# Kernel tuning notes

Hardware: AMD Instinct MI355X
Metric: run time of the kernel (lower is better)

Reference implementation:

```python
import jax, jax.numpy as jnp
import numpy as np

EMBED_DIM = 128
WINDOW_SIZE = 128
B, S, D = 2, 2048, EMBED_DIM
NEG_INF = -1e9


def setup_inputs() -> dict:
    key = jax.random.key(0)
    kq, kk, kv = jax.random.split(key, 3)
    q = jax.random.normal(kq, (B, S, D), dtype=jnp.float32)
    k = jax.random.normal(kk, (B, S, D), dtype=jnp.float32)
    v = jax.random.normal(kv, (B, S, D), dtype=jnp.float32)
    return {"q": q, "k": k, "v": v}


def reference(q, k, v):
    # Sliding-window causal attention: token i attends to [i-W, i] inclusive.
    Bq, Sq, Dq = q.shape
    W = WINDOW_SIZE
    scale = Dq ** -0.5
    offsets = jnp.arange(-W, 1)                      # [W+1]
    idx = jnp.arange(Sq)[:, None] + offsets[None, :]  # [S, W+1]
    valid = idx >= 0                                  # mask out-of-range (pre-sequence) keys
    idx_c = jnp.clip(idx, 0, Sq - 1)
    k_win = k[:, idx_c]                               # [B, S, W+1, D]
    v_win = v[:, idx_c]                               # [B, S, W+1, D]
    scores = jnp.einsum('bsd,bswd->bsw', q, k_win) * scale
    scores = jnp.where(valid[None, :, :], scores, NEG_INF)
    attn = jax.nn.softmax(scores, axis=-1)            # [B, S, W+1]
    out = jnp.einsum('bsw,bswd->bsd', attn, v_win)    # [B, S, D]
    return out
```

## Files before the change

### kernel.cpp

```cpp
#include <hip/hip_runtime.h>
#include <hip/hip_bf16.h>
#include <math.h>

#define SEQ 2048
#define DIME 128
#define BQ 16
#define NEG_INF -1.0e9f

typedef __attribute__((ext_vector_type(8))) short bf16x8;
typedef __attribute__((ext_vector_type(4))) float f32x4;

static __device__ __forceinline__ short cvt(float x) {
  __hip_bfloat16 h(x);
  return __builtin_bit_cast(short, h);
}

static __device__ __forceinline__ bf16x8 pack8(const float4 lo, const float4 hi) {
  bf16x8 f;
  f[0] = cvt(lo.x); f[1] = cvt(lo.y); f[2] = cvt(lo.z); f[3] = cvt(lo.w);
  f[4] = cvt(hi.x); f[5] = cvt(hi.y); f[6] = cvt(hi.z); f[7] = cvt(hi.w);
  return f;
}

__global__ __launch_bounds__(256) void swa_kernel(
    const float* __restrict__ q, const float* __restrict__ k,
    const float* __restrict__ v, float* __restrict__ out) {
  __shared__ float P[16][180];
  __shared__ float mW[9][16];
  __shared__ float sW[9][16];

  const int tid = threadIdx.x;
  const int lane = tid & 63;
  const int w = tid >> 6;
  const int col = lane & 15;
  const int g = lane >> 4;

  const int blk = blockIdx.x;
  const int b = blk >> 7;
  const int qs = (blk & 127) * BQ;
  const int kbase = qs - 128;

  const float* __restrict__ qb = q + (size_t)b * SEQ * DIME;
  const float* __restrict__ kb = k + (size_t)b * SEQ * DIME;
  const float* __restrict__ vb = v + (size_t)b * SEQ * DIME;

  float4 qlo[4], qhi[4];
  {
    const float* qrow = qb + (size_t)(qs + col) * DIME + 8 * g;
#pragma unroll
    for (int kc = 0; kc < 4; ++kc) {
      qlo[kc] = *(const float4*)(qrow + 32 * kc);
      qhi[kc] = *(const float4*)(qrow + 32 * kc + 4);
    }
  }

  float4 kraw[3][8];
#pragma unroll
  for (int ti = 0; ti < 2; ++ti) {
    const int t = 2 * w + ti;
    int krow = kbase + 16 * t + col;
    krow = krow < 0 ? 0 : krow;
    const float* krp = kb + (size_t)krow * DIME + 8 * g;
#pragma unroll
    for (int kc = 0; kc < 4; ++kc) {
      kraw[ti][2 * kc]     = *(const float4*)(krp + 32 * kc);
      kraw[ti][2 * kc + 1] = *(const float4*)(krp + 32 * kc + 4);
    }
  }
  if (w == 0) {
    const int krow = kbase + 16 * 8 + col;
    const float* krp = kb + (size_t)krow * DIME + 8 * g;
#pragma unroll
    for (int kc = 0; kc < 4; ++kc) {
      kraw[2][2 * kc]     = *(const float4*)(krp + 32 * kc);
      kraw[2][2 * kc + 1] = *(const float4*)(krp + 32 * kc + 4);
    }
  }

  float2 vv[5][8];
#pragma unroll
  for (int c = 0; c < 5; ++c)
#pragma unroll
    for (int j = 0; j < 8; ++j) {
      int kg = kbase + 32 * c + 8 * g + j;
      kg = kg < 0 ? 0 : (kg > SEQ - 1 ? SEQ - 1 : kg);
      vv[c][j] = *(const float2*)(vb + (size_t)kg * DIME + 32 * w + 2 * col);
    }

  P[tid >> 4][144 + (tid & 15)] = 0.f;

  bf16x8 qf[4];
#pragma unroll
  for (int kc = 0; kc < 4; ++kc) qf[kc] = pack8(qlo[kc], qhi[kc]);

  const float scale = 0.08838834764831845f;
  auto process = [&](int t, const float4 (&raw)[8]) {
    f32x4 acc = {0.f, 0.f, 0.f, 0.f};
#pragma unroll
    for (int kc = 0; kc < 4; ++kc)
      acc = __builtin_amdgcn_mfma_f32_16x16x32_bf16(
          pack8(raw[2 * kc], raw[2 * kc + 1]), qf[kc], acc, 0, 0, 0);
    float sc[4];
    float m = NEG_INF;
#pragma unroll
    for (int r = 0; r < 4; ++r) {
      const int kg = kbase + 16 * t + 4 * g + r;
      const int qg = qs + col;
      const bool valid = (kg >= 0) && (kg >= qg - 128) && (kg <= qg);
      sc[r] = valid ? acc[r] * scale : NEG_INF;
      m = fmaxf(m, sc[r]);
    }
    m = fmaxf(m, __shfl_xor(m, 16));
    m = fmaxf(m, __shfl_xor(m, 32));
    float s = 0.f;
#pragma unroll
    for (int r = 0; r < 4; ++r) { sc[r] = __expf(sc[r] - m); s += sc[r]; }
    s += __shfl_xor(s, 16);
    s += __shfl_xor(s, 32);
    if (g == 0) { mW[t][col] = m; sW[t][col] = s; }
    const float4 scv = {sc[0], sc[1], sc[2], sc[3]};
    *(float4*)&P[col][16 * t + 4 * g] = scv;
  };
  process(2 * w, kraw[0]);
  process(2 * w + 1, kraw[1]);
  if (w == 0) process(8, kraw[2]);

  __syncthreads();

  float M = mW[0][col];
#pragma unroll
  for (int t = 1; t < 9; ++t) M = fmaxf(M, mW[t][col]);
  float e[9], St = 0.f;
#pragma unroll
  for (int t = 0; t < 9; ++t) {
    e[t] = __expf(mW[t][col] - M);
    St += sW[t][col] * e[t];
  }
  const float inv = 1.0f / St;
  float swt[5];
#pragma unroll
  for (int c = 0; c < 5; ++c) {
    const float ehi = (2 * c + 1 < 9) ? e[2 * c + 1] : 0.f;
    swt[c] = ((g >> 1) ? ehi : e[2 * c]) * inv;
  }

  f32x4 o0 = {0.f, 0.f, 0.f, 0.f}, o1 = {0.f, 0.f, 0.f, 0.f};
#pragma unroll
  for (int c = 0; c < 5; ++c) {
    const float4 pA = *(const float4*)&P[col][32 * c + 8 * g];
    const float4 pB = *(const float4*)&P[col][32 * c + 8 * g + 4];
    bf16x8 pa, b0, b1;
    pa[0] = cvt(pA.x * swt[c]); pa[1] = cvt(pA.y * swt[c]);
    pa[2] = cvt(pA.z * swt[c]); pa[3] = cvt(pA.w * swt[c]);
    pa[4] = cvt(pB.x * swt[c]); pa[5] = cvt(pB.y * swt[c]);
    pa[6] = cvt(pB.z * swt[c]); pa[7] = cvt(pB.w * swt[c]);
#pragma unroll
    for (int j = 0; j < 8; ++j) {
      b0[j] = cvt(vv[c][j].x);
      b1[j] = cvt(vv[c][j].y);
    }
    o0 = __builtin_amdgcn_mfma_f32_16x16x32_bf16(pa, b0, o0, 0, 0, 0);
    o1 = __builtin_amdgcn_mfma_f32_16x16x32_bf16(pa, b1, o1, 0, 0, 0);
  }

#pragma unroll
  for (int r = 0; r < 4; ++r) {
    const int qrow = 4 * g + r;
    float2 val = {o0[r], o1[r]};
    *(float2*)&out[(size_t)(b * SEQ + qs + qrow) * DIME + 32 * w + 2 * col] = val;
  }
}

extern "C" void kernel_launch(void* const* d_in, const int* in_sizes, int n_in,
                              void* d_out, int out_size, void* d_ws, size_t ws_size,
                              hipStream_t stream) {
  const float* q = (const float*)d_in[0];
  const float* k = (const float*)d_in[1];
  const float* v = (const float*)d_in[2];
  float* out = (float*)d_out;
  dim3 grid(256), block(256);
  swa_kernel<<<grid, block, 0, stream>>>(q, k, v, out);
}
```

Before: 12.38 us.

## Stage V tile through swizzled LDS with coalesced float4 loads and remap blocks

V rows are now loaded with fully coalesced float4 global reads into a padded, XOR-swizzled shared-memory tile. Each wave then gathers its MFMA B-operand values from LDS, replacing the strided float2 global loads. The output column mapping changes so each MFMA result writes a contiguous 16-float segment. Block indices are permuted so neighbouring tiles land on different XCDs/CUs. Together these aim to improve global memory efficiency, at the cost of about 84KB of extra LDS, which limits blocks per CU, plus many scalar LDS reads.

```diff
diff --git a/kernel.cpp b/kernel.cpp
--- a/kernel.cpp
+++ b/kernel.cpp
@@ -22,10 +22,15 @@
   return f;
 }
 
+static __device__ __forceinline__ int vaddr(int row, int dim) {
+  return row * 132 + (dim ^ (((row >> 3) & 3) << 4));
+}
+
 __global__ __launch_bounds__(256) void swa_kernel(
     const float* __restrict__ q, const float* __restrict__ k,
     const float* __restrict__ v, float* __restrict__ out) {
   __shared__ float P[16][180];
+  __shared__ float Vlds[160 * 132];
   __shared__ float mW[9][16];
   __shared__ float sW[9][16];
 
@@ -35,14 +40,25 @@
   const int col = lane & 15;
   const int g = lane >> 4;
 
-  const int blk = blockIdx.x;
-  const int b = blk >> 7;
-  const int qs = (blk & 127) * BQ;
+  const int phys = blockIdx.x;
+  const int tile = (phys & 7) * 32 + (phys >> 3);
+  const int b = tile >> 7;
+  const int qs = (tile & 127) * BQ;
   const int kbase = qs - 128;
 
   const float* __restrict__ qb = q + (size_t)b * SEQ * DIME;
   const float* __restrict__ kb = k + (size_t)b * SEQ * DIME;
   const float* __restrict__ vb = v + (size_t)b * SEQ * DIME;
+
+  const int vrow0 = 40 * w + (lane >> 5);
+  const int vdim = 4 * (lane & 31);
+  float4 vst[20];
+#pragma unroll
+  for (int i = 0; i < 20; ++i) {
+    int kg = kbase + vrow0 + 2 * i;
+    kg = kg < 0 ? 0 : (kg > SEQ - 1 ? SEQ - 1 : kg);
+    vst[i] = *(const float4*)(vb + (size_t)kg * DIME + vdim);
+  }
 
   float4 qlo[4], qhi[4];
   {
@@ -77,15 +93,9 @@
     }
   }
 
-  float2 vv[5][8];
 #pragma unroll
-  for (int c = 0; c < 5; ++c)
-#pragma unroll
-    for (int j = 0; j < 8; ++j) {
-      int kg = kbase + 32 * c + 8 * g + j;
-      kg = kg < 0 ? 0 : (kg > SEQ - 1 ? SEQ - 1 : kg);
-      vv[c][j] = *(const float2*)(vb + (size_t)kg * DIME + 32 * w + 2 * col);
-    }
+  for (int i = 0; i < 20; ++i)
+    *(float4*)&Vlds[vaddr(vrow0 + 2 * i, vdim)] = vst[i];
 
   P[tid >> 4][144 + (tid & 15)] = 0.f;
 
@@ -156,8 +166,9 @@
     pa[6] = cvt(pB.z * swt[c]); pa[7] = cvt(pB.w * swt[c]);
 #pragma unroll
     for (int j = 0; j < 8; ++j) {
-      b0[j] = cvt(vv[c][j].x);
-      b1[j] = cvt(vv[c][j].y);
+      const int slot = 32 * c + 8 * g + j;
+      b0[j] = cvt(Vlds[vaddr(slot, 32 * w + col)]);
+      b1[j] = cvt(Vlds[vaddr(slot, 32 * w + 16 + col)]);
     }
     o0 = __builtin_amdgcn_mfma_f32_16x16x32_bf16(pa, b0, o0, 0, 0, 0);
     o1 = __builtin_amdgcn_mfma_f32_16x16x32_bf16(pa, b1, o1, 0, 0, 0);
@@ -166,8 +177,9 @@
 #pragma unroll
   for (int r = 0; r < 4; ++r) {
     const int qrow = 4 * g + r;
-    float2 val = {o0[r], o1[r]};
-    *(float2*)&out[(size_t)(b * SEQ + qs + qrow) * DIME + 32 * w + 2 * col] = val;
+    float* op = out + (size_t)(b * SEQ + qs + qrow) * DIME + 32 * w;
+    op[col] = o0[r];
+    op[16 + col] = o1[r];
   }
 }
 
```

After: 12.31 us. About the same (-0.6%).
